# Optimization experiments

Hardware: AMD Instinct MI355X
Metric: run time of the kernel (lower is better)

## Reference

```python
import jax, jax.numpy as jnp
import numpy as np

HIDDEN = 128
INPUT_DIM = 1
NUM_CLASSES = 2


def setup_inputs() -> dict:
    key = jax.random.key(0)
    ks = jax.random.split(key, 7)
    B, T = 256, 1024
    s_ih = 1.0 / np.sqrt(HIDDEN)
    x = jax.random.normal(ks[0], (B, T, INPUT_DIM), dtype=jnp.float32)
    W_ih = jax.random.uniform(ks[1], (HIDDEN, INPUT_DIM), jnp.float32, -s_ih, s_ih)
    W_hh = jax.random.uniform(ks[2], (HIDDEN, HIDDEN), jnp.float32, -s_ih, s_ih)
    b_ih = jax.random.uniform(ks[3], (HIDDEN,), jnp.float32, -s_ih, s_ih)
    b_hh = jax.random.uniform(ks[4], (HIDDEN,), jnp.float32, -s_ih, s_ih)
    W_fc = jax.random.uniform(ks[5], (NUM_CLASSES, HIDDEN), jnp.float32, -s_ih, s_ih)
    b_fc = jax.random.uniform(ks[6], (NUM_CLASSES,), jnp.float32, -s_ih, s_ih)
    return {"x": x, "W_ih": W_ih, "W_hh": W_hh, "b_ih": b_ih,
            "b_hh": b_hh, "W_fc": W_fc, "b_fc": b_fc}


def reference(x, W_ih, W_hh, b_ih, b_hh, W_fc, b_fc):
    B = x.shape[0]
    # Precompute input projection for all timesteps: [B,T,H]
    xp = jnp.einsum('bti,hi->bth', x, W_ih) + b_ih + b_hh
    h0 = jnp.zeros((B, HIDDEN), dtype=x.dtype)

    def step(h, xp_t):
        h_new = jnp.tanh(xp_t + h @ W_hh.T)  # [B,H]
        return h_new, h_new

    _, hs = jax.lax.scan(step, h0, jnp.swapaxes(xp, 0, 1))  # hs: [T,B,H]
    out = jnp.swapaxes(hs, 0, 1)  # [B,T,H]
    logits = jnp.einsum('bth,ch->btc', out, W_fc) + b_fc  # [B,T,C]
    return logits
```

## Files before the change

kernel.cpp:

```cpp
#include <hip/hip_runtime.h>

typedef float f32x2 __attribute__((ext_vector_type(2)));
typedef float f32x4 __attribute__((ext_vector_type(4)));

#define BB 256
#define TT 1024
#define HH 128
#define CC 2
#define NG 2

__device__ __forceinline__ float ftanh(float u) {
    float e = __expf(2.0f * u);
    float r = __builtin_amdgcn_rcpf(e + 1.0f);
    return fmaf(-2.0f, r, 1.0f);
}

__device__ __forceinline__ float bcast(float v, int j) {
    return __int_as_float(__builtin_amdgcn_readlane(__float_as_int(v), j));
}

#define DPP_ADD(v, ctrl)                                                     \
    ((v) + __int_as_float(__builtin_amdgcn_mov_dpp(                          \
         __float_as_int(v), (ctrl), 0xF, 0xF, true)))

__global__ __launch_bounds__(512, 2) void rnn_kernel(
    const float* __restrict__ x, const float* __restrict__ W_ih,
    const float* __restrict__ W_hh, const float* __restrict__ b_ih,
    const float* __restrict__ b_hh, const float* __restrict__ W_fc,
    const float* __restrict__ b_fc, float* __restrict__ out)
{
    const int b   = blockIdx.x;
    const int tid = threadIdx.x;
    const int g   = tid >> 8;
    const int t2  = tid & 255;
    const int l   = tid & 63;
    const int wv  = (tid >> 6) & 3;
    const int lq  = l & 31;
    const int kb  = wv << 5;
    const int rA  = l, rB = l + 64;
    const int rF  = kb + lq;

    __shared__ float xs[NG][TT + 8];
    __shared__ f32x2 p2[2][NG][4][64];
    __shared__ f32x2 qp[4][NG][4];

    {
        const f32x4* xr = (const f32x4*)(x + (size_t)(NG * b + g) * TT);
        ((f32x4*)xs[g])[t2] = xr[t2];
    }
    if (t2 < 8) xs[g][TT + t2] = 0.f;

    const float wih  = W_ih[rF];
    const float bias = b_ih[rF] + b_hh[rF];
    const float wfs  = (l < 32) ? W_fc[rF] : W_fc[HH + rF];
    const float bf0  = b_fc[0], bf1 = b_fc[1];

    float wa[32], wb[32];
    {
        const f32x4* a4 = (const f32x4*)(W_hh + (size_t)rA * HH + kb);
        const f32x4* b4 = (const f32x4*)(W_hh + (size_t)rB * HH + kb);
        #pragma unroll
        for (int j = 0; j < 8; ++j) {
            f32x4 va = a4[j], vb = b4[j];
            wa[4*j+0] = va.x; wa[4*j+1] = va.y; wa[4*j+2] = va.z; wa[4*j+3] = va.w;
            wb[4*j+0] = vb.x; wb[4*j+1] = vb.y; wb[4*j+2] = vb.z; wb[4*j+3] = vb.w;
        }
    }

    float hn = 0.f;
    float* o = out + (size_t)(NG * b + g) * TT * CC;

    __syncthreads();
    float xcur = xs[g][0];

    #pragma unroll 4
    for (int t = 0; t < TT; ++t) {
        const int buf = t & 1, qb = t & 3;

        float aA0 = 0.f, aA1 = 0.f, aB0 = 0.f, aB1 = 0.f;
        #pragma unroll
        for (int k = 0; k < 32; k += 2) {
            float s0 = bcast(hn, k);
            float s1 = bcast(hn, k + 1);
            aA0 = fmaf(wa[k],     s0, aA0);
            aB0 = fmaf(wb[k],     s0, aB0);
            aA1 = fmaf(wa[k + 1], s1, aA1);
            aB1 = fmaf(wb[k + 1], s1, aB1);
        }
        f32x2 pr = { aA0 + aA1, aB0 + aB1 };
        p2[buf][g][wv][l] = pr;

        {
            float q = wfs * hn;
            q = DPP_ADD(q, 0xB1);
            q = DPP_ADD(q, 0x4E);
            q = DPP_ADD(q, 0x124);
            q = DPP_ADD(q, 0x128);
            float q0 = bcast(q, 0)  + bcast(q, 16);
            float q1 = bcast(q, 32) + bcast(q, 48);
            if (l == 0) qp[qb][g][wv] = f32x2{q0, q1};
        }

        const float base  = fmaf(xcur, wih, bias);
        const float xnext = xs[g][t + 1];

        __syncthreads();

        if (t > 0 && t2 == 0) {
            f32x2 s = (qp[qb][g][0] + qp[qb][g][1]) + (qp[qb][g][2] + qp[qb][g][3]);
            s.x += bf0; s.y += bf1;
            *(f32x2*)(o + (t - 1) * CC) = s;
        }

        const float* pf = (const float*)&p2[buf][g][0][0]
                        + ((((wv & 1) << 5) + lq) << 1) + (wv >> 1);
        float p0 = pf[0], p1 = pf[128], pv2 = pf[256], pv3 = pf[384];
        hn = ftanh(base + ((p0 + p1) + (pv2 + pv3)));
        xcur = xnext;
    }

    {
        float q = wfs * hn;
        q = DPP_ADD(q, 0xB1);
        q = DPP_ADD(q, 0x4E);
        q = DPP_ADD(q, 0x124);
        q = DPP_ADD(q, 0x128);
        float q0 = bcast(q, 0)  + bcast(q, 16);
        float q1 = bcast(q, 32) + bcast(q, 48);
        if (l == 0) qp[0][g][wv] = f32x2{q0, q1};
    }
    __syncthreads();
    if (t2 == 0) {
        f32x2 s = (qp[0][g][0] + qp[0][g][1]) + (qp[0][g][2] + qp[0][g][3]);
        s.x += bf0; s.y += bf1;
        *(f32x2*)(o + (TT - 1) * CC) = s;
    }
}

extern "C" void kernel_launch(void* const* d_in, const int* in_sizes, int n_in,
                              void* d_out, int out_size, void* d_ws, size_t ws_size,
                              hipStream_t stream) {
    const float* x    = (const float*)d_in[0];
    const float* W_ih = (const float*)d_in[1];
    const float* W_hh = (const float*)d_in[2];
    const float* b_ih = (const float*)d_in[3];
    const float* b_hh = (const float*)d_in[4];
    const float* W_fc = (const float*)d_in[5];
    const float* b_fc = (const float*)d_in[6];
    float* out = (float*)d_out;

    rnn_kernel<<<BB / NG, 512, 0, stream>>>(x, W_ih, W_hh, b_ih, b_hh, W_fc, b_fc, out);
}
```

Before: 540.6 us.

## Stagger the two batch groups half a step apart to overlap matvec and reduce phases

The two sequences in a block now run out of phase: while group 0 does the matvec/broadcast phase, group 1 does the reduction and tanh phase, and they swap after each barrier. Each timestep now costs two block barriers instead of one. The aim is to interleave the two groups' latency-bound phases so each barrier interval holds mixed work. Launch bounds drop to one block per CU, which relaxes register limits but may reduce occupancy.

```diff
diff --git a/kernel.cpp b/kernel.cpp
--- a/kernel.cpp
+++ b/kernel.cpp
@@ -23,7 +23,7 @@
     ((v) + __int_as_float(__builtin_amdgcn_mov_dpp(                          \
          __float_as_int(v), (ctrl), 0xF, 0xF, true)))
 
-__global__ __launch_bounds__(512, 2) void rnn_kernel(
+__global__ __launch_bounds__(512, 1) void rnn_kernel(
     const float* __restrict__ x, const float* __restrict__ W_ih,
     const float* __restrict__ W_hh, const float* __restrict__ b_ih,
     const float* __restrict__ b_hh, const float* __restrict__ W_fc,
@@ -67,57 +67,61 @@
         }
     }
 
-    float hn = 0.f;
+    float hn = 0.f, base = 0.f;
     float* o = out + (size_t)(NG * b + g) * TT * CC;
 
     __syncthreads();
     float xcur = xs[g][0];
 
-    #pragma unroll 4
+#define H1(T) {                                                              \
+        const int buf_ = (T) & 1, qb_ = (T) & 3;                             \
+        float aA0 = 0.f, aA1 = 0.f, aB0 = 0.f, aB1 = 0.f;                    \
+        _Pragma("unroll")                                                    \
+        for (int k = 0; k < 32; k += 2) {                                    \
+            float s0 = bcast(hn, k);                                         \
+            float s1 = bcast(hn, k + 1);                                     \
+            aA0 = fmaf(wa[k],     s0, aA0);                                  \
+            aB0 = fmaf(wb[k],     s0, aB0);                                  \
+            aA1 = fmaf(wa[k + 1], s1, aA1);                                  \
+            aB1 = fmaf(wb[k + 1], s1, aB1);                                  \
+        }                                                                    \
+        f32x2 pr = { aA0 + aA1, aB0 + aB1 };                                 \
+        p2[buf_][g][wv][l] = pr;                                             \
+        float q = wfs * hn;                                                  \
+        q = DPP_ADD(q, 0xB1);                                                \
+        q = DPP_ADD(q, 0x4E);                                                \
+        q = DPP_ADD(q, 0x124);                                               \
+        q = DPP_ADD(q, 0x128);                                               \
+        float q0 = bcast(q, 0)  + bcast(q, 16);                              \
+        float q1 = bcast(q, 32) + bcast(q, 48);                              \
+        if (l == 0) qp[qb_][g][wv] = f32x2{q0, q1};                          \
+        base = fmaf(xcur, wih, bias);                                        \
+        xcur = xs[g][(T) + 1];                                               \
+    }
+
+#define H2(T) {                                                              \
+        const int buf_ = (T) & 1, qb_ = (T) & 3;                             \
+        if ((T) > 0 && t2 == 0) {                                            \
+            f32x2 s = (qp[qb_][g][0] + qp[qb_][g][1])                        \
+                    + (qp[qb_][g][2] + qp[qb_][g][3]);                       \
+            s.x += bf0; s.y += bf1;                                          \
+            *(f32x2*)(o + ((T) - 1) * CC) = s;                               \
+        }                                                                    \
+        const float* pf = (const float*)&p2[buf_][g][0][0]                   \
+                        + ((((wv & 1) << 5) + lq) << 1) + (wv >> 1);         \
+        float p0 = pf[0], p1 = pf[128], pv2 = pf[256], pv3 = pf[384];        \
+        hn = ftanh(base + ((p0 + p1) + (pv2 + pv3)));                        \
+    }
+
+    #pragma unroll 2
     for (int t = 0; t < TT; ++t) {
-        const int buf = t & 1, qb = t & 3;
+        if (g == 0) { H1(t) } else if (t > 0) { H2(t - 1) }
+        __syncthreads();
+        if (g == 0) { H2(t) } else { H1(t) }
+        __syncthreads();
+    }
 
-        float aA0 = 0.f, aA1 = 0.f, aB0 = 0.f, aB1 = 0.f;
-        #pragma unroll
-        for (int k = 0; k < 32; k += 2) {
-            float s0 = bcast(hn, k);
-            float s1 = bcast(hn, k + 1);
-            aA0 = fmaf(wa[k],     s0, aA0);
-            aB0 = fmaf(wb[k],     s0, aB0);
-            aA1 = fmaf(wa[k + 1], s1, aA1);
-            aB1 = fmaf(wb[k + 1], s1, aB1);
-        }
-        f32x2 pr = { aA0 + aA1, aB0 + aB1 };
-        p2[buf][g][wv][l] = pr;
-
-        {
-            float q = wfs * hn;
-            q = DPP_ADD(q, 0xB1);
-            q = DPP_ADD(q, 0x4E);
-            q = DPP_ADD(q, 0x124);
-            q = DPP_ADD(q, 0x128);
-            float q0 = bcast(q, 0)  + bcast(q, 16);
-            float q1 = bcast(q, 32) + bcast(q, 48);
-            if (l == 0) qp[qb][g][wv] = f32x2{q0, q1};
-        }
-
-        const float base  = fmaf(xcur, wih, bias);
-        const float xnext = xs[g][t + 1];
-
-        __syncthreads();
-
-        if (t > 0 && t2 == 0) {
-            f32x2 s = (qp[qb][g][0] + qp[qb][g][1]) + (qp[qb][g][2] + qp[qb][g][3]);
-            s.x += bf0; s.y += bf1;
-            *(f32x2*)(o + (t - 1) * CC) = s;
-        }
-
-        const float* pf = (const float*)&p2[buf][g][0][0]
-                        + ((((wv & 1) << 5) + lq) << 1) + (wv >> 1);
-        float p0 = pf[0], p1 = pf[128], pv2 = pf[256], pv3 = pf[384];
-        hn = ftanh(base + ((p0 + p1) + (pv2 + pv3)));
-        xcur = xnext;
-    }
+    if (g == 1) { H2(TT - 1) }
 
     {
         float q = wfs * hn;
@@ -135,6 +139,8 @@
         s.x += bf0; s.y += bf1;
         *(f32x2*)(o + (TT - 1) * CC) = s;
     }
+#undef H1
+#undef H2
 }
 
 extern "C" void kernel_launch(void* const* d_in, const int* in_sizes, int n_in,
```

New measurement: 705.0 us. 30.4% more time.
